# Performance work log

Measured on AMD Instinct MI355X. Metric: run time of the kernel, lower is better.

## Reference

```python
import jax, jax.numpy as jnp
import numpy as np


def _linear(x, W, b):
    # torch nn.Linear: y = x @ W.T + b, W is [out, in]
    return x @ W.T + b


def _sage_layer(x, edge_index, Ws, bs, Wn, bn):
    # GraphSAGE: mean-aggregate neighbor features via scatter-add, then two linears.
    src, tgt = edge_index[0], edge_index[1]
    N = x.shape[0]
    agg = jax.ops.segment_sum(x[src], tgt, num_segments=N)            # [N, D]
    deg = jax.ops.segment_sum(jnp.ones(src.shape, x.dtype), tgt, num_segments=N)  # [N]
    neighbor_mean = agg / jnp.maximum(deg, 1.0)[:, None]
    return _linear(x, Ws, bs) + _linear(neighbor_mean, Wn, bn)


def setup_inputs() -> dict:
    key = jax.random.key(0)
    ks = jax.random.split(key, 16)
    N, ATTR, H, OUT, E = 50000, 125, 128, 128, 800000
    IN = ATTR + 3
    s = 0.05
    inp = {
        "attr_features": jax.random.normal(ks[0], (N, ATTR), jnp.float32),
        "clustering_coefficient": jax.random.uniform(ks[1], (N, 1), jnp.float32),
        "bidirectional_links_ratio": jax.random.uniform(ks[2], (N, 1), jnp.float32),
        "exist_nodes": jnp.ones((N,), jnp.float32),
        "W_in": s * jax.random.normal(ks[3], (H, IN), jnp.float32),
        "b_in": s * jax.random.normal(ks[4], (H,), jnp.float32),
        "W1_self": s * jax.random.normal(ks[5], (H, H), jnp.float32),
        "b1_self": s * jax.random.normal(ks[6], (H,), jnp.float32),
        "W1_neigh": s * jax.random.normal(ks[7], (H, H), jnp.float32),
        "b1_neigh": s * jax.random.normal(ks[8], (H,), jnp.float32),
        "W2_self": s * jax.random.normal(ks[9], (OUT, H), jnp.float32),
        "b2_self": s * jax.random.normal(ks[10], (OUT,), jnp.float32),
        "W2_neigh": s * jax.random.normal(ks[11], (OUT, H), jnp.float32),
        "b2_neigh": s * jax.random.normal(ks[12], (OUT,), jnp.float32),
        "edge_index": jax.random.randint(ks[13], (2, E), 0, N, jnp.int64),
    }
    return inp


def reference(attr_features, clustering_coefficient, bidirectional_links_ratio,
              exist_nodes, W_in, b_in, W1_self, b1_self, W1_neigh, b1_neigh,
              W2_self, b2_self, W2_neigh, b2_neigh, edge_index):
    exist_col = exist_nodes[:, None]                                   # [N, 1]
    x = jnp.concatenate(
        [attr_features, clustering_coefficient, bidirectional_links_ratio, exist_col],
        axis=1)                                                        # [N, attr_dim+3]
    x = jax.nn.relu(_linear(x, W_in, b_in))                            # dropout=0 -> identity
    x = _sage_layer(x, edge_index, W1_self, b1_self, W1_neigh, b1_neigh)
    x = jax.nn.relu(x)
    x = x * exist_col
    x = _sage_layer(x, edge_index, W2_self, b2_self, W2_neigh, b2_neigh)
    return x * exist_col
```

## Files before the change

kernel.cpp:

```cpp
#include <hip/hip_runtime.h>

typedef __attribute__((ext_vector_type(8))) short short8;
typedef __attribute__((ext_vector_type(4))) float floatx4;

__device__ inline unsigned short f2bf(float f) {
    unsigned u = __float_as_uint(f);
    u += 0x7fffu + ((u >> 16) & 1u);
    return (unsigned short)(u >> 16);
}

#define CHUNK_CAP 12288
#define BTILE 4096
#define NPREP 256


__global__ __launch_bounds__(256, 3) void gemm0_bin(
    const float* __restrict__ attr, const float* __restrict__ cc,
    const float* __restrict__ bl, const float* __restrict__ ex,
    const float* __restrict__ Wf, const float* __restrict__ bias,
    unsigned short* __restrict__ out_bf,
    const int* __restrict__ e, int* __restrict__ cursor,
    unsigned* __restrict__ packed_out,
    const float* __restrict__ w1s, const float* __restrict__ w1n,
    const float* __restrict__ w2s, const float* __restrict__ w2n,
    const float* __restrict__ b1s, const float* __restrict__ b1n,
    const float* __restrict__ b2s, const float* __restrict__ b2n,
    unsigned short* __restrict__ wb, float* __restrict__ biasf,
    int N, int ATTR, int E, int ntilesE, int nbin) {
    __shared__ __align__(16) char smem[49408];
    int t = threadIdx.x;
    int bid = blockIdx.x;

    if (bid < nbin) {
        unsigned* buf  = (unsigned*)smem;
        unsigned* sbuf = buf + BTILE;
        int* hist  = (int*)(sbuf + BTILE);
        int* offs  = hist + 128;
        int* gbase = offs + 128;
        int* lcur  = gbase + 128;
        for (int tile = bid; tile < ntilesE; tile += nbin) {
            int e0 = tile * BTILE;
            int cnt = min(BTILE, E - e0);
            if (t < 128) hist[t] = 0;
            __syncthreads();
            for (int j = t; j < cnt; j += 256) {
                unsigned src = (unsigned)e[e0 + j];
                unsigned tgt = (unsigned)e[E + e0 + j];
                unsigned c = tgt >> 9;
                buf[j] = (c << 25) | (src << 9) | (tgt & 511u);
                atomicAdd(&hist[c], 1);
            }
            __syncthreads();
            if (t < 128) offs[t] = hist[t];
            __syncthreads();
            for (int o = 1; o < 128; o <<= 1) {
                int v = (t < 128 && t >= o) ? offs[t - o] : 0;
                __syncthreads();
                if (t < 128) offs[t] += v;
                __syncthreads();
            }
            if (t < 128) {
                int excl = offs[t] - hist[t];
                offs[t] = excl;
                lcur[t] = excl;
                gbase[t] = (hist[t] > 0) ? t * CHUNK_CAP + atomicAdd(&cursor[t], hist[t]) : 0;
            }
            __syncthreads();
            for (int j = t; j < cnt; j += 256) {
                unsigned v = buf[j];
                int c = v >> 25;
                int p = atomicAdd(&lcur[c], 1);
                sbuf[p] = v;
            }
            __syncthreads();
            int wv = t >> 6, lane = t & 63;
            for (int c = wv; c < 128; c += 4) {
                int n = hist[c], lo = offs[c], gb = gbase[c];
                for (int j = lane; j < n; j += 64)
                    packed_out[gb + j] = sbuf[lo + j];
            }
            __syncthreads();
        }
        return;
    }

    if (bid < nbin + NPREP) {
        int pb = bid - nbin;
        int idx = pb * 256 + t;
        int m = idx >> 14, j = idx & 16383;
        const float* src = (m == 0) ? w1s : (m == 1) ? w1n : (m == 2) ? w2s : w2n;
        wb[idx] = f2bf(src[j]);
        if (pb == 0 && t < 128) {
            biasf[t]       = b1s[t] + b1n[t];
            biasf[128 + t] = b2s[t] + b2n[t];
        }
        return;
    }

    float* sflat = (float*)smem;
    unsigned short* lx = (unsigned short*)(smem + 32000);
    int lane = t & 63;
    int w = t >> 6;
    int node0 = (bid - nbin - NPREP) * 64;
    int n_off = w * 32;
    int q = lane >> 4;
    int m16 = lane & 15;

    int nrow = N - node0; nrow = nrow > 64 ? 64 : (nrow < 0 ? 0 : nrow);
    int nelem = nrow * ATTR;
    {
        const float* abase = attr + (size_t)node0 * ATTR;
        int nv = nelem >> 2;
        const float4* src4 = (const float4*)abase;
        for (int i = t; i < nv; i += 256) ((float4*)sflat)[i] = src4[i];
        for (int i = (nv << 2) + t; i < nelem; i += 256) sflat[i] = abase[i];
    }

    short8 bf[2][4];
    #pragma unroll
    for (int nt = 0; nt < 2; ++nt)
        #pragma unroll
        for (int kk = 0; kk < 4; ++kk) {
            const float* p = Wf + (n_off + nt * 16 + m16) * 128 + kk * 32 + q * 8;
            float4 aa = *(const float4*)p, bb = *(const float4*)(p + 4);
            short8 r;
            r[0] = (short)f2bf(aa.x); r[1] = (short)f2bf(aa.y);
            r[2] = (short)f2bf(aa.z); r[3] = (short)f2bf(aa.w);
            r[4] = (short)f2bf(bb.x); r[5] = (short)f2bf(bb.y);
            r[6] = (short)f2bf(bb.z); r[7] = (short)f2bf(bb.w);
            bf[nt][kk] = r;
        }

    floatx4 acc[4][2];
    #pragma unroll
    for (int nt = 0; nt < 2; ++nt) {
        float bv = bias[n_off + nt * 16 + m16];
        floatx4 b4 = {bv, bv, bv, bv};
        #pragma unroll
        for (int mt = 0; mt < 4; ++mt) acc[mt][nt] = b4;
    }
    __syncthreads();

    for (int i = 0; i < 32; ++i) {
        int idx = t + 256 * i;
        int nd = idx >> 7, col = idx & 127;
        int row = node0 + nd;
        float v = 0.0f;
        if (row < N) {
            if (col < ATTR)           v = sflat[nd * ATTR + col];
            else if (col == ATTR)     v = cc[row];
            else if (col == ATTR + 1) v = bl[row];
            else                      v = ex[row];
        }
        lx[nd * 136 + col] = f2bf(v);
    }
    __syncthreads();

    #pragma unroll
    for (int kk = 0; kk < 4; ++kk) {
        short8 a[4];
        #pragma unroll
        for (int mt = 0; mt < 4; ++mt)
            a[mt] = *(const short8*)(lx + (mt * 16 + m16) * 136 + kk * 32 + q * 8);
        #pragma unroll
        for (int mt = 0; mt < 4; ++mt) {
            acc[mt][0] = __builtin_amdgcn_mfma_f32_16x16x32_bf16(a[mt], bf[0][kk], acc[mt][0], 0, 0, 0);
            acc[mt][1] = __builtin_amdgcn_mfma_f32_16x16x32_bf16(a[mt], bf[1][kk], acc[mt][1], 0, 0, 0);
        }
    }

    for (int mt = 0; mt < 4; ++mt) {
        int rbase = node0 + mt * 16 + q * 4;
        for (int r = 0; r < 4; ++r) {
            int rr = rbase + r;
            if (rr >= N) continue;
            for (int nt = 0; nt < 2; ++nt) {
                float v = fmaxf(acc[mt][nt][r], 0.0f);
                out_bf[(size_t)rr * 128 + n_off + nt * 16 + m16] = f2bf(v);
            }
        }
    }
}


__global__ __launch_bounds__(256) void chunk_csr(const unsigned* __restrict__ packed,
                                                 const int* __restrict__ cursor,
                                                 uint2* __restrict__ rows2,
                                                 int* __restrict__ colv, int N) {
    __shared__ int hist[512], offs[512], lcnt[512], pp[256];
    __shared__ int sbuf[CHUNK_CAP];
    int c = blockIdx.x;
    int base = c * CHUNK_CAP;
    int cnt = cursor[c];
    int t = threadIdx.x;
    hist[t] = 0;
    hist[t + 256] = 0;
    __syncthreads();
    for (int j = t; j < cnt; j += 256)
        atomicAdd(&hist[packed[base + j] & 511u], 1);
    __syncthreads();
    int a0 = hist[2 * t], a1 = hist[2 * t + 1];
    pp[t] = a0 + a1;
    __syncthreads();
    for (int o = 1; o < 256; o <<= 1) {
        int v = (t >= o) ? pp[t - o] : 0;
        __syncthreads();
        pp[t] += v;
        __syncthreads();
    }
    int excl = pp[t] - (a0 + a1);
    offs[2 * t] = excl;
    offs[2 * t + 1] = excl + a0;
    lcnt[2 * t] = 0;
    lcnt[2 * t + 1] = 0;
    __syncthreads();
    for (int j = t; j < 512; j += 256) {
        int node = c * 512 + j;
        if (node < N) {
            uint2 r;
            r.x = base + offs[j];
            r.y = base + offs[j] + hist[j];
            rows2[node] = r;
        }
    }
    for (int j = t; j < cnt; j += 256) {
        unsigned v = packed[base + j];
        int node = v & 511u;
        int p = offs[node] + atomicAdd(&lcnt[node], 1);
        sbuf[p] = (v >> 9) & 0xFFFFu;
    }
    __syncthreads();
    for (int j = t; j < cnt; j += 256) colv[base + j] = sbuf[j];
}


__global__ __launch_bounds__(256) void agg_mean(const unsigned short* __restrict__ x,
                                                const uint2* __restrict__ rows2,
                                                const int* __restrict__ colv,
                                                unsigned short* __restrict__ nm, int N) {
    int wid = (blockIdx.x * 256 + threadIdx.x) >> 6;
    int lane = threadIdx.x & 63;
    if (wid >= N) return;
    uint2 r = rows2[wid];
    int s0 = r.x, s1 = r.y;
    int deg = s1 - s0;
    int mn = deg < 64 ? deg : 64;
    int cvec = (lane < mn) ? colv[s0 + lane] : 0;
    int quarter = lane >> 4;
    int cl = (lane & 15) * 8;
    float a0 = 0.f, a1 = 0.f, a2 = 0.f, a3 = 0.f;
    float a4 = 0.f, a5 = 0.f, a6 = 0.f, a7 = 0.f;
    int lim = mn - 1;
    for (int j = 0; j < mn; j += 32) {
        uint4 v[8];
        #pragma unroll
        for (int u = 0; u < 8; ++u) {
            int ei = j + 4 * u + quarter;
            int idx = (ei <= lim) ? ei : lim;
            int s = __shfl(cvec, idx, 64);
            v[u] = *(const uint4*)(x + (size_t)s * 128 + cl);
        }
        #pragma unroll
        for (int u = 0; u < 8; ++u) {
            int ei = j + 4 * u + quarter;
            if (ei <= lim) {
                a0 += __uint_as_float(v[u].x << 16);
                a1 += __uint_as_float(v[u].x & 0xffff0000u);
                a2 += __uint_as_float(v[u].y << 16);
                a3 += __uint_as_float(v[u].y & 0xffff0000u);
                a4 += __uint_as_float(v[u].z << 16);
                a5 += __uint_as_float(v[u].z & 0xffff0000u);
                a6 += __uint_as_float(v[u].w << 16);
                a7 += __uint_as_float(v[u].w & 0xffff0000u);
            }
        }
    }
    for (int e = s0 + 64; e < s1; e += 4) {
        int ei = e + quarter;
        int idx = (ei < s1) ? ei : s1 - 1;
        int s = colv[idx];
        uint4 v = *(const uint4*)(x + (size_t)s * 128 + cl);
        if (ei < s1) {
            a0 += __uint_as_float(v.x << 16);
            a1 += __uint_as_float(v.x & 0xffff0000u);
            a2 += __uint_as_float(v.y << 16);
            a3 += __uint_as_float(v.y & 0xffff0000u);
            a4 += __uint_as_float(v.z << 16);
            a5 += __uint_as_float(v.z & 0xffff0000u);
            a6 += __uint_as_float(v.w << 16);
            a7 += __uint_as_float(v.w & 0xffff0000u);
        }
    }
    a0 += __shfl_xor(a0, 16, 64); a0 += __shfl_xor(a0, 32, 64);
    a1 += __shfl_xor(a1, 16, 64); a1 += __shfl_xor(a1, 32, 64);
    a2 += __shfl_xor(a2, 16, 64); a2 += __shfl_xor(a2, 32, 64);
    a3 += __shfl_xor(a3, 16, 64); a3 += __shfl_xor(a3, 32, 64);
    a4 += __shfl_xor(a4, 16, 64); a4 += __shfl_xor(a4, 32, 64);
    a5 += __shfl_xor(a5, 16, 64); a5 += __shfl_xor(a5, 32, 64);
    a6 += __shfl_xor(a6, 16, 64); a6 += __shfl_xor(a6, 32, 64);
    a7 += __shfl_xor(a7, 16, 64); a7 += __shfl_xor(a7, 32, 64);
    if (quarter == 0) {
        float inv = 1.0f / (float)(deg > 1 ? deg : 1);
        a0 *= inv; a1 *= inv; a2 *= inv; a3 *= inv;
        a4 *= inv; a5 *= inv; a6 *= inv; a7 *= inv;
        uint4 o;
        o.x = ((unsigned)f2bf(a1) << 16) | (unsigned)f2bf(a0);
        o.y = ((unsigned)f2bf(a3) << 16) | (unsigned)f2bf(a2);
        o.z = ((unsigned)f2bf(a5) << 16) | (unsigned)f2bf(a4);
        o.w = ((unsigned)f2bf(a7) << 16) | (unsigned)f2bf(a6);
        *(uint4*)(nm + (size_t)wid * 128 + cl) = o;
    }
}


__global__ __launch_bounds__(256, 3) void gemm_fused(
    const unsigned short* __restrict__ X0, const unsigned short* __restrict__ X1,
    const unsigned short* __restrict__ W0, const unsigned short* __restrict__ W1,
    const float* __restrict__ bias, const float* __restrict__ ex,
    unsigned short* __restrict__ obf, float* __restrict__ of32,
    int N, int relu) {
    __shared__ unsigned short lx[64 * 136];
    int tid = threadIdx.x;
    int lane = tid & 63;
    int w = tid >> 6;
    int node0 = blockIdx.x * 64;
    int n_off = w * 32;
    int q = lane >> 4;
    int m16 = lane & 15;

    short8 bf0[2][4], bf1[2][4];
    #pragma unroll
    for (int nt = 0; nt < 2; ++nt)
        #pragma unroll
        for (int kk = 0; kk < 4; ++kk) {
            bf0[nt][kk] = *(const short8*)(W0 + (n_off + nt * 16 + m16) * 128 + kk * 32 + q * 8);
            bf1[nt][kk] = *(const short8*)(W1 + (n_off + nt * 16 + m16) * 128 + kk * 32 + q * 8);
        }

    floatx4 acc[4][2];
    #pragma unroll
    for (int nt = 0; nt < 2; ++nt) {
        float bv = bias[n_off + nt * 16 + m16];
        floatx4 b4 = {bv, bv, bv, bv};
        #pragma unroll
        for (int mt = 0; mt < 4; ++mt) acc[mt][nt] = b4;
    }

    for (int ph = 0; ph < 2; ++ph) {
        const unsigned short* X = ph ? X1 : X0;
        for (int i = 0; i < 4; ++i) {
            int c = tid + 256 * i;
            int nd = c >> 4, ck = c & 15;
            short8 v = {0, 0, 0, 0, 0, 0, 0, 0};
            if (node0 + nd < N) v = *(const short8*)(X + (size_t)(node0 + nd) * 128 + ck * 8);
            *(short8*)(lx + nd * 136 + ck * 8) = v;
        }
        __syncthreads();
        #pragma unroll
        for (int kk = 0; kk < 4; ++kk) {
            short8 a[4];
            #pragma unroll
            for (int mt = 0; mt < 4; ++mt)
                a[mt] = *(const short8*)(lx + (mt * 16 + m16) * 136 + kk * 32 + q * 8);
            #pragma unroll
            for (int mt = 0; mt < 4; ++mt) {
                const short8* p0 = ph ? &bf1[0][kk] : &bf0[0][kk];
                const short8* p1 = ph ? &bf1[1][kk] : &bf0[1][kk];
                acc[mt][0] = __builtin_amdgcn_mfma_f32_16x16x32_bf16(a[mt], *p0, acc[mt][0], 0, 0, 0);
                acc[mt][1] = __builtin_amdgcn_mfma_f32_16x16x32_bf16(a[mt], *p1, acc[mt][1], 0, 0, 0);
            }
        }
        __syncthreads();
    }

    for (int mt = 0; mt < 4; ++mt) {
        int rbase = node0 + mt * 16 + q * 4;
        for (int r = 0; r < 4; ++r) {
            int rr = rbase + r;
            if (rr >= N) continue;
            float e = ex ? ex[rr] : 1.0f;
            for (int nt = 0; nt < 2; ++nt) {
                float v = acc[mt][nt][r];
                if (relu) v = fmaxf(v, 0.0f);
                v *= e;
                int col = n_off + nt * 16 + m16;
                if (obf) obf[(size_t)rr * 128 + col] = f2bf(v);
                else     of32[(size_t)rr * 128 + col] = v;
            }
        }
    }
}


extern "C" void kernel_launch(void* const* d_in, const int* in_sizes, int n_in,
                              void* d_out, int out_size, void* d_ws, size_t ws_size,
                              hipStream_t stream) {
    const float* attr = (const float*)d_in[0];
    const float* cc   = (const float*)d_in[1];
    const float* bl   = (const float*)d_in[2];
    const float* ex   = (const float*)d_in[3];
    const float* w_in = (const float*)d_in[4];
    const float* b_in = (const float*)d_in[5];
    const float* w1s  = (const float*)d_in[6];
    const float* b1s  = (const float*)d_in[7];
    const float* w1n  = (const float*)d_in[8];
    const float* b1n  = (const float*)d_in[9];
    const float* w2s  = (const float*)d_in[10];
    const float* b2s  = (const float*)d_in[11];
    const float* w2n  = (const float*)d_in[12];
    const float* b2n  = (const float*)d_in[13];
    const int*   eidx = (const int*)d_in[14];

    int N = in_sizes[3];
    int ATTR = in_sizes[0] / N;
    int E = in_sizes[14] / 2;
    int Npad = ((N + 63) / 64) * 64;
    int nchunk = (N + 511) / 512;
    int ntilesE = (E + BTILE - 1) / BTILE;
    int nbin = ntilesE < 256 ? ntilesE : 256;
    int gblk = Npad / 64;

    char* ws = (char*)d_ws;
    size_t off = 0;
    auto alloc = [&](size_t bytes) -> char* {
        off = (off + 255) & ~(size_t)255;
        char* p = ws + off;
        off += bytes;
        return p;
    };
    unsigned short* x1 = (unsigned short*)alloc((size_t)Npad * 128 * 2);
    unsigned short* x2 = (unsigned short*)alloc((size_t)Npad * 128 * 2);
    unsigned short* nm = (unsigned short*)alloc((size_t)Npad * 128 * 2);
    int* colv        = (int*)alloc((size_t)nchunk * CHUNK_CAP * 4);
    unsigned* packed = (unsigned*)alloc((size_t)nchunk * CHUNK_CAP * 4);
    uint2* rows2     = (uint2*)alloc((size_t)N * 8);
    int* cursor      = (int*)alloc(128 * 4);
    unsigned short* wb = (unsigned short*)alloc((size_t)4 * 16384 * 2);
    float* biasf     = (float*)alloc(256 * 4);

    hipMemsetAsync(cursor, 0, 128 * sizeof(int), stream);

    gemm0_bin<<<nbin + NPREP + gblk, 256, 0, stream>>>(
        attr, cc, bl, ex, w_in, b_in, x1,
        eidx, cursor, packed,
        w1s, w1n, w2s, w2n, b1s, b1n, b2s, b2n, wb, biasf,
        N, ATTR, E, ntilesE, nbin);
    chunk_csr<<<nchunk, 256, 0, stream>>>(packed, cursor, rows2, colv, N);
    agg_mean<<<(N + 3) / 4, 256, 0, stream>>>(x1, rows2, colv, nm, N);
    gemm_fused<<<gblk, 256, 0, stream>>>(x1, nm, wb, wb + 16384,
                                         biasf, ex, x2, (float*)nullptr, N, 1);
    agg_mean<<<(N + 3) / 4, 256, 0, stream>>>(x2, rows2, colv, nm, N);
    gemm_fused<<<gblk, 256, 0, stream>>>(x2, nm, wb + 2 * 16384, wb + 3 * 16384,
                                         biasf + 128, ex, (unsigned short*)nullptr,
                                         (float*)d_out, N, 0);
}
```

Baseline: 242.1 us.

## Fuse CSR build into front kernel and fuse neighbor aggregation into SAGE GEMMs

The chunk_csr pass moves into the front kernel, with CSR blocks spin-waiting on a global done counter set by the binning blocks. Binning now uses one 2048-edge tile per block instead of a grid-stride loop. Mean aggregation is computed inside each SAGE GEMM block straight into shared memory, which drops the nm buffer and three launches. The input GEMM now loads attr directly with vectorised loads, and outputs are staged through LDS for coalesced stores. The spin-wait relies on binning blocks being scheduled before the waiting blocks and adds some deadlock and ordering risk.

```diff
diff --git a/kernel.cpp b/kernel.cpp
--- a/kernel.cpp
+++ b/kernel.cpp
@@ -10,82 +10,134 @@
 }
 
 #define CHUNK_CAP 12288
-#define BTILE 4096
+#define BTILE 2048
 #define NPREP 256
 
 
-__global__ __launch_bounds__(256, 3) void gemm0_bin(
+__global__ __launch_bounds__(256, 4) void front_fused(
     const float* __restrict__ attr, const float* __restrict__ cc,
     const float* __restrict__ bl, const float* __restrict__ ex,
-    const float* __restrict__ Wf, const float* __restrict__ bias,
-    unsigned short* __restrict__ out_bf,
-    const int* __restrict__ e, int* __restrict__ cursor,
+    const float* __restrict__ Wf, const float* __restrict__ bias0,
+    unsigned short* __restrict__ x1,
+    const int* __restrict__ e, int* __restrict__ cursor, int* __restrict__ done,
     unsigned* __restrict__ packed_out,
+    uint2* __restrict__ rows2, int* __restrict__ colv,
     const float* __restrict__ w1s, const float* __restrict__ w1n,
     const float* __restrict__ w2s, const float* __restrict__ w2n,
     const float* __restrict__ b1s, const float* __restrict__ b1n,
     const float* __restrict__ b2s, const float* __restrict__ b2n,
     unsigned short* __restrict__ wb, float* __restrict__ biasf,
-    int N, int ATTR, int E, int ntilesE, int nbin) {
-    __shared__ __align__(16) char smem[49408];
+    int N, int ATTR, int E, int ntilesE, int nchunk) {
+    __shared__ __align__(16) char smem[18432];
     int t = threadIdx.x;
     int bid = blockIdx.x;
 
-    if (bid < nbin) {
+    if (bid < ntilesE) {
         unsigned* buf  = (unsigned*)smem;
         unsigned* sbuf = buf + BTILE;
         int* hist  = (int*)(sbuf + BTILE);
         int* offs  = hist + 128;
         int* gbase = offs + 128;
         int* lcur  = gbase + 128;
-        for (int tile = bid; tile < ntilesE; tile += nbin) {
-            int e0 = tile * BTILE;
-            int cnt = min(BTILE, E - e0);
-            if (t < 128) hist[t] = 0;
+        int e0 = bid * BTILE;
+        int cnt = min(BTILE, E - e0);
+        if (t < 128) hist[t] = 0;
+        __syncthreads();
+        for (int j = t; j < cnt; j += 256) {
+            unsigned src = (unsigned)e[e0 + j];
+            unsigned tgt = (unsigned)e[E + e0 + j];
+            unsigned c = tgt >> 9;
+            buf[j] = (c << 25) | (src << 9) | (tgt & 511u);
+            atomicAdd(&hist[c], 1);
+        }
+        __syncthreads();
+        if (t < 128) offs[t] = hist[t];
+        __syncthreads();
+        for (int o = 1; o < 128; o <<= 1) {
+            int v = (t < 128 && t >= o) ? offs[t - o] : 0;
             __syncthreads();
-            for (int j = t; j < cnt; j += 256) {
-                unsigned src = (unsigned)e[e0 + j];
-                unsigned tgt = (unsigned)e[E + e0 + j];
-                unsigned c = tgt >> 9;
-                buf[j] = (c << 25) | (src << 9) | (tgt & 511u);
-                atomicAdd(&hist[c], 1);
-            }
+            if (t < 128) offs[t] += v;
             __syncthreads();
-            if (t < 128) offs[t] = hist[t];
+        }
+        if (t < 128) {
+            int excl = offs[t] - hist[t];
+            offs[t] = excl;
+            lcur[t] = excl;
+            gbase[t] = (hist[t] > 0) ? t * CHUNK_CAP + atomicAdd(&cursor[t], hist[t]) : 0;
+        }
+        __syncthreads();
+        for (int j = t; j < cnt; j += 256) {
+            unsigned v = buf[j];
+            int c = v >> 25;
+            int p = atomicAdd(&lcur[c], 1);
+            sbuf[p] = v;
+        }
+        __syncthreads();
+        for (int j = t; j < cnt; j += 256) {
+            unsigned v = sbuf[j];
+            int c = v >> 25;
+            packed_out[gbase[c] + (j - offs[c])] = v;
+        }
+        __threadfence();
+        __syncthreads();
+        if (t == 0) atomicAdd(done, 1);
+        return;
+    }
+
+    if (bid < ntilesE + nchunk) {
+        int* hist = (int*)smem;
+        int* offs = hist + 512;
+        int* lcnt = offs + 512;
+        int* pp   = lcnt + 512;
+        int c = bid - ntilesE;
+        if (t == 0) {
+            while (atomicAdd(done, 0) < ntilesE) __builtin_amdgcn_s_sleep(8);
+            __threadfence();
+        }
+        __syncthreads();
+        int base = c * CHUNK_CAP;
+        int cnt = atomicAdd(&cursor[c], 0);
+        hist[t] = 0;
+        hist[t + 256] = 0;
+        __syncthreads();
+        for (int j = t; j < cnt; j += 256)
+            atomicAdd(&hist[packed_out[base + j] & 511u], 1);
+        __syncthreads();
+        int a0 = hist[2 * t], a1 = hist[2 * t + 1];
+        pp[t] = a0 + a1;
+        __syncthreads();
+        for (int o = 1; o < 256; o <<= 1) {
+            int v = (t >= o) ? pp[t - o] : 0;
             __syncthreads();
-            for (int o = 1; o < 128; o <<= 1) {
-                int v = (t < 128 && t >= o) ? offs[t - o] : 0;
-                __syncthreads();
-                if (t < 128) offs[t] += v;
-                __syncthreads();
-            }
-            if (t < 128) {
-                int excl = offs[t] - hist[t];
-                offs[t] = excl;
-                lcur[t] = excl;
-                gbase[t] = (hist[t] > 0) ? t * CHUNK_CAP + atomicAdd(&cursor[t], hist[t]) : 0;
-            }
+            pp[t] += v;
             __syncthreads();
-            for (int j = t; j < cnt; j += 256) {
-                unsigned v = buf[j];
-                int c = v >> 25;
-                int p = atomicAdd(&lcur[c], 1);
-                sbuf[p] = v;
-            }
-            __syncthreads();
-            int wv = t >> 6, lane = t & 63;
-            for (int c = wv; c < 128; c += 4) {
-                int n = hist[c], lo = offs[c], gb = gbase[c];
-                for (int j = lane; j < n; j += 64)
-                    packed_out[gb + j] = sbuf[lo + j];
-            }
-            __syncthreads();
+        }
+        int excl = pp[t] - (a0 + a1);
+        offs[2 * t] = excl;
+        offs[2 * t + 1] = excl + a0;
+        lcnt[2 * t] = 0;
+        lcnt[2 * t + 1] = 0;
+        __syncthreads();
+        for (int j = t; j < 512; j += 256) {
+            int node = c * 512 + j;
+            if (node < N) {
+                uint2 r;
+                r.x = base + offs[j];
+                r.y = base + offs[j] + hist[j];
+                rows2[node] = r;
+            }
+        }
+        for (int j = t; j < cnt; j += 256) {
+            unsigned v = packed_out[base + j];
+            int node = v & 511u;
+            int p = offs[node] + atomicAdd(&lcnt[node], 1);
+            colv[base + p] = (v >> 9) & 0xFFFFu;
         }
         return;
     }
 
-    if (bid < nbin + NPREP) {
-        int pb = bid - nbin;
+    if (bid < ntilesE + nchunk + NPREP) {
+        int pb = bid - ntilesE - nchunk;
         int idx = pb * 256 + t;
         int m = idx >> 14, j = idx & 16383;
         const float* src = (m == 0) ? w1s : (m == 1) ? w1n : (m == 2) ? w2s : w2n;
@@ -97,24 +149,13 @@
         return;
     }
 
-    float* sflat = (float*)smem;
-    unsigned short* lx = (unsigned short*)(smem + 32000);
+    unsigned short* lx = (unsigned short*)smem;
     int lane = t & 63;
     int w = t >> 6;
-    int node0 = (bid - nbin - NPREP) * 64;
+    int node0 = (bid - ntilesE - nchunk - NPREP) * 64;
     int n_off = w * 32;
     int q = lane >> 4;
     int m16 = lane & 15;
-
-    int nrow = N - node0; nrow = nrow > 64 ? 64 : (nrow < 0 ? 0 : nrow);
-    int nelem = nrow * ATTR;
-    {
-        const float* abase = attr + (size_t)node0 * ATTR;
-        int nv = nelem >> 2;
-        const float4* src4 = (const float4*)abase;
-        for (int i = t; i < nv; i += 256) ((float4*)sflat)[i] = src4[i];
-        for (int i = (nv << 2) + t; i < nelem; i += 256) sflat[i] = abase[i];
-    }
 
     short8 bf[2][4];
     #pragma unroll
@@ -134,25 +175,45 @@
     floatx4 acc[4][2];
     #pragma unroll
     for (int nt = 0; nt < 2; ++nt) {
-        float bv = bias[n_off + nt * 16 + m16];
+        float bv = bias0[n_off + nt * 16 + m16];
         floatx4 b4 = {bv, bv, bv, bv};
         #pragma unroll
         for (int mt = 0; mt < 4; ++mt) acc[mt][nt] = b4;
     }
-    __syncthreads();
-
-    for (int i = 0; i < 32; ++i) {
+
+    if (node0 + 64 > N) {
+        for (int i = t; i < 64 * 136; i += 256) lx[i] = 0;
+        __syncthreads();
+    }
+
+    #pragma unroll
+    for (int i = 0; i < 8; ++i) {
         int idx = t + 256 * i;
-        int nd = idx >> 7, col = idx & 127;
+        int nd = idx >> 5, g = idx & 31;
         int row = node0 + nd;
-        float v = 0.0f;
-        if (row < N) {
-            if (col < ATTR)           v = sflat[nd * ATTR + col];
-            else if (col == ATTR)     v = cc[row];
-            else if (col == ATTR + 1) v = bl[row];
-            else                      v = ex[row];
-        }
-        lx[nd * 136 + col] = f2bf(v);
+        int c0 = g * 4;
+        if (row < N && c0 < ATTR) {
+            if (c0 + 3 < ATTR) {
+                float4 f = *(const float4*)(attr + (size_t)row * ATTR + c0);
+                unsigned lo = (unsigned)f2bf(f.x) | ((unsigned)f2bf(f.y) << 16);
+                unsigned hi = (unsigned)f2bf(f.z) | ((unsigned)f2bf(f.w) << 16);
+                uint2 pk; pk.x = lo; pk.y = hi;
+                *(uint2*)(lx + nd * 136 + c0) = pk;
+            } else {
+                for (int k = 0; k < 4; ++k) {
+                    int cidx = c0 + k;
+                    if (cidx < ATTR) lx[nd * 136 + cidx] = f2bf(attr[(size_t)row * ATTR + cidx]);
+                }
+            }
+        }
+    }
+    {
+        int nd = t >> 2, ci = t & 3;
+        int row = node0 + nd;
+        if (ci < 3 && row < N) {
+            float v = (ci == 0) ? cc[row] : (ci == 1) ? bl[row] : ex[row];
+            lx[nd * 136 + ATTR + ci] = f2bf(v);
+        }
     }
     __syncthreads();
 
@@ -169,160 +230,41 @@
         }
     }
 
-    for (int mt = 0; mt < 4; ++mt) {
-        int rbase = node0 + mt * 16 + q * 4;
+    __syncthreads();
+    #pragma unroll
+    for (int mt = 0; mt < 4; ++mt)
+        #pragma unroll
         for (int r = 0; r < 4; ++r) {
-            int rr = rbase + r;
-            if (rr >= N) continue;
-            for (int nt = 0; nt < 2; ++nt) {
-                float v = fmaxf(acc[mt][nt][r], 0.0f);
-                out_bf[(size_t)rr * 128 + n_off + nt * 16 + m16] = f2bf(v);
-            }
-        }
+            int rl = mt * 16 + q * 4 + r;
+            #pragma unroll
+            for (int nt = 0; nt < 2; ++nt)
+                lx[rl * 136 + n_off + nt * 16 + m16] = f2bf(fmaxf(acc[mt][nt][r], 0.0f));
+        }
+    __syncthreads();
+    #pragma unroll
+    for (int i = 0; i < 4; ++i) {
+        int cidx = t + 256 * i;
+        int nd = cidx >> 4, k = cidx & 15;
+        int rr = node0 + nd;
+        if (rr < N)
+            *(uint4*)(x1 + (size_t)rr * 128 + k * 8) = *(const uint4*)(lx + nd * 136 + k * 8);
     }
 }
 
 
-__global__ __launch_bounds__(256) void chunk_csr(const unsigned* __restrict__ packed,
-                                                 const int* __restrict__ cursor,
-                                                 uint2* __restrict__ rows2,
-                                                 int* __restrict__ colv, int N) {
-    __shared__ int hist[512], offs[512], lcnt[512], pp[256];
-    __shared__ int sbuf[CHUNK_CAP];
-    int c = blockIdx.x;
-    int base = c * CHUNK_CAP;
-    int cnt = cursor[c];
-    int t = threadIdx.x;
-    hist[t] = 0;
-    hist[t + 256] = 0;
-    __syncthreads();
-    for (int j = t; j < cnt; j += 256)
-        atomicAdd(&hist[packed[base + j] & 511u], 1);
-    __syncthreads();
-    int a0 = hist[2 * t], a1 = hist[2 * t + 1];
-    pp[t] = a0 + a1;
-    __syncthreads();
-    for (int o = 1; o < 256; o <<= 1) {
-        int v = (t >= o) ? pp[t - o] : 0;
-        __syncthreads();
-        pp[t] += v;
-        __syncthreads();
-    }
-    int excl = pp[t] - (a0 + a1);
-    offs[2 * t] = excl;
-    offs[2 * t + 1] = excl + a0;
-    lcnt[2 * t] = 0;
-    lcnt[2 * t + 1] = 0;
-    __syncthreads();
-    for (int j = t; j < 512; j += 256) {
-        int node = c * 512 + j;
-        if (node < N) {
-            uint2 r;
-            r.x = base + offs[j];
-            r.y = base + offs[j] + hist[j];
-            rows2[node] = r;
-        }
-    }
-    for (int j = t; j < cnt; j += 256) {
-        unsigned v = packed[base + j];
-        int node = v & 511u;
-        int p = offs[node] + atomicAdd(&lcnt[node], 1);
-        sbuf[p] = (v >> 9) & 0xFFFFu;
-    }
-    __syncthreads();
-    for (int j = t; j < cnt; j += 256) colv[base + j] = sbuf[j];
-}
-
-
-__global__ __launch_bounds__(256) void agg_mean(const unsigned short* __restrict__ x,
-                                                const uint2* __restrict__ rows2,
-                                                const int* __restrict__ colv,
-                                                unsigned short* __restrict__ nm, int N) {
-    int wid = (blockIdx.x * 256 + threadIdx.x) >> 6;
-    int lane = threadIdx.x & 63;
-    if (wid >= N) return;
-    uint2 r = rows2[wid];
-    int s0 = r.x, s1 = r.y;
-    int deg = s1 - s0;
-    int mn = deg < 64 ? deg : 64;
-    int cvec = (lane < mn) ? colv[s0 + lane] : 0;
-    int quarter = lane >> 4;
-    int cl = (lane & 15) * 8;
-    float a0 = 0.f, a1 = 0.f, a2 = 0.f, a3 = 0.f;
-    float a4 = 0.f, a5 = 0.f, a6 = 0.f, a7 = 0.f;
-    int lim = mn - 1;
-    for (int j = 0; j < mn; j += 32) {
-        uint4 v[8];
-        #pragma unroll
-        for (int u = 0; u < 8; ++u) {
-            int ei = j + 4 * u + quarter;
-            int idx = (ei <= lim) ? ei : lim;
-            int s = __shfl(cvec, idx, 64);
-            v[u] = *(const uint4*)(x + (size_t)s * 128 + cl);
-        }
-        #pragma unroll
-        for (int u = 0; u < 8; ++u) {
-            int ei = j + 4 * u + quarter;
-            if (ei <= lim) {
-                a0 += __uint_as_float(v[u].x << 16);
-                a1 += __uint_as_float(v[u].x & 0xffff0000u);
-                a2 += __uint_as_float(v[u].y << 16);
-                a3 += __uint_as_float(v[u].y & 0xffff0000u);
-                a4 += __uint_as_float(v[u].z << 16);
-                a5 += __uint_as_float(v[u].z & 0xffff0000u);
-                a6 += __uint_as_float(v[u].w << 16);
-                a7 += __uint_as_float(v[u].w & 0xffff0000u);
-            }
-        }
-    }
-    for (int e = s0 + 64; e < s1; e += 4) {
-        int ei = e + quarter;
-        int idx = (ei < s1) ? ei : s1 - 1;
-        int s = colv[idx];
-        uint4 v = *(const uint4*)(x + (size_t)s * 128 + cl);
-        if (ei < s1) {
-            a0 += __uint_as_float(v.x << 16);
-            a1 += __uint_as_float(v.x & 0xffff0000u);
-            a2 += __uint_as_float(v.y << 16);
-            a3 += __uint_as_float(v.y & 0xffff0000u);
-            a4 += __uint_as_float(v.z << 16);
-            a5 += __uint_as_float(v.z & 0xffff0000u);
-            a6 += __uint_as_float(v.w << 16);
-            a7 += __uint_as_float(v.w & 0xffff0000u);
-        }
-    }
-    a0 += __shfl_xor(a0, 16, 64); a0 += __shfl_xor(a0, 32, 64);
-    a1 += __shfl_xor(a1, 16, 64); a1 += __shfl_xor(a1, 32, 64);
-    a2 += __shfl_xor(a2, 16, 64); a2 += __shfl_xor(a2, 32, 64);
-    a3 += __shfl_xor(a3, 16, 64); a3 += __shfl_xor(a3, 32, 64);
-    a4 += __shfl_xor(a4, 16, 64); a4 += __shfl_xor(a4, 32, 64);
-    a5 += __shfl_xor(a5, 16, 64); a5 += __shfl_xor(a5, 32, 64);
-    a6 += __shfl_xor(a6, 16, 64); a6 += __shfl_xor(a6, 32, 64);
-    a7 += __shfl_xor(a7, 16, 64); a7 += __shfl_xor(a7, 32, 64);
-    if (quarter == 0) {
-        float inv = 1.0f / (float)(deg > 1 ? deg : 1);
-        a0 *= inv; a1 *= inv; a2 *= inv; a3 *= inv;
-        a4 *= inv; a5 *= inv; a6 *= inv; a7 *= inv;
-        uint4 o;
-        o.x = ((unsigned)f2bf(a1) << 16) | (unsigned)f2bf(a0);
-        o.y = ((unsigned)f2bf(a3) << 16) | (unsigned)f2bf(a2);
-        o.z = ((unsigned)f2bf(a5) << 16) | (unsigned)f2bf(a4);
-        o.w = ((unsigned)f2bf(a7) << 16) | (unsigned)f2bf(a6);
-        *(uint4*)(nm + (size_t)wid * 128 + cl) = o;
-    }
-}
-
-
-__global__ __launch_bounds__(256, 3) void gemm_fused(
-    const unsigned short* __restrict__ X0, const unsigned short* __restrict__ X1,
+__global__ __launch_bounds__(256, 3) void gemm_sage(
+    const unsigned short* __restrict__ X,
+    const uint2* __restrict__ rows2, const int* __restrict__ colv,
     const unsigned short* __restrict__ W0, const unsigned short* __restrict__ W1,
     const float* __restrict__ bias, const float* __restrict__ ex,
     unsigned short* __restrict__ obf, float* __restrict__ of32,
     int N, int relu) {
-    __shared__ unsigned short lx[64 * 136];
-    int tid = threadIdx.x;
-    int lane = tid & 63;
-    int w = tid >> 6;
+    __shared__ __align__(16) char smem[34816];
+    unsigned short* lxA = (unsigned short*)smem;
+    unsigned short* lxB = lxA + 64 * 136;
+    int t = threadIdx.x;
+    int lane = t & 63;
+    int w = t >> 6;
     int node0 = blockIdx.x * 64;
     int n_off = w * 32;
     int q = lane >> 4;
@@ -346,47 +288,163 @@
         for (int mt = 0; mt < 4; ++mt) acc[mt][nt] = b4;
     }
 
-    for (int ph = 0; ph < 2; ++ph) {
-        const unsigned short* X = ph ? X1 : X0;
+    #pragma unroll
+    for (int i = 0; i < 4; ++i) {
+        int c = t + 256 * i;
+        int nd = c >> 4, ck = c & 15;
+        short8 v = {0, 0, 0, 0, 0, 0, 0, 0};
+        if (node0 + nd < N) v = *(const short8*)(X + (size_t)(node0 + nd) * 128 + ck * 8);
+        *(short8*)(lxA + nd * 136 + ck * 8) = v;
+    }
+
+    int cl = m16 * 8;
+    for (int i = 0; i < 16; ++i) {
+        int row = w * 16 + i;
+        int node = node0 + row;
+        int s0 = 0, s1 = 0;
+        if (node < N) { uint2 r2 = rows2[node]; s0 = r2.x; s1 = r2.y; }
+        int deg = s1 - s0;
+        int mn = deg < 64 ? deg : 64;
+        int cvec = (lane < mn) ? colv[s0 + lane] : 0;
+        float a0 = 0.f, a1 = 0.f, a2 = 0.f, a3 = 0.f;
+        float a4 = 0.f, a5 = 0.f, a6 = 0.f, a7 = 0.f;
+        int lim = mn - 1;
+        for (int j = 0; j < mn; j += 32) {
+            uint4 v[8];
+            #pragma unroll
+            for (int u = 0; u < 8; ++u) {
+                int ei = j + 4 * u + q;
+                int idx = (ei <= lim) ? ei : lim;
+                int s = __shfl(cvec, idx, 64);
+                v[u] = *(const uint4*)(X + (size_t)s * 128 + cl);
+            }
+            #pragma unroll
+            for (int u = 0; u < 8; ++u) {
+                int ei = j + 4 * u + q;
+                if (ei <= lim) {
+                    a0 += __uint_as_float(v[u].x << 16);
+                    a1 += __uint_as_float(v[u].x & 0xffff0000u);
+                    a2 += __uint_as_float(v[u].y << 16);
+                    a3 += __uint_as_float(v[u].y & 0xffff0000u);
+                    a4 += __uint_as_float(v[u].z << 16);
+                    a5 += __uint_as_float(v[u].z & 0xffff0000u);
+                    a6 += __uint_as_float(v[u].w << 16);
+                    a7 += __uint_as_float(v[u].w & 0xffff0000u);
+                }
+            }
+        }
+        for (int eo = s0 + 64; eo < s1; eo += 4) {
+            int ei = eo + q;
+            int idx = (ei < s1) ? ei : s1 - 1;
+            int s = colv[idx];
+            uint4 v = *(const uint4*)(X + (size_t)s * 128 + cl);
+            if (ei < s1) {
+                a0 += __uint_as_float(v.x << 16);
+                a1 += __uint_as_float(v.x & 0xffff0000u);
+                a2 += __uint_as_float(v.y << 16);
+                a3 += __uint_as_float(v.y & 0xffff0000u);
+                a4 += __uint_as_float(v.z << 16);
+                a5 += __uint_as_float(v.z & 0xffff0000u);
+                a6 += __uint_as_float(v.w << 16);
+                a7 += __uint_as_float(v.w & 0xffff0000u);
+            }
+        }
+        a0 += __shfl_xor(a0, 16, 64); a0 += __shfl_xor(a0, 32, 64);
+        a1 += __shfl_xor(a1, 16, 64); a1 += __shfl_xor(a1, 32, 64);
+        a2 += __shfl_xor(a2, 16, 64); a2 += __shfl_xor(a2, 32, 64);
+        a3 += __shfl_xor(a3, 16, 64); a3 += __shfl_xor(a3, 32, 64);
+        a4 += __shfl_xor(a4, 16, 64); a4 += __shfl_xor(a4, 32, 64);
+        a5 += __shfl_xor(a5, 16, 64); a5 += __shfl_xor(a5, 32, 64);
+        a6 += __shfl_xor(a6, 16, 64); a6 += __shfl_xor(a6, 32, 64);
+        a7 += __shfl_xor(a7, 16, 64); a7 += __shfl_xor(a7, 32, 64);
+        if (q == 0) {
+            float inv = 1.0f / (float)(deg > 1 ? deg : 1);
+            a0 *= inv; a1 *= inv; a2 *= inv; a3 *= inv;
+            a4 *= inv; a5 *= inv; a6 *= inv; a7 *= inv;
+            uint4 o;
+            o.x = ((unsigned)f2bf(a1) << 16) | (unsigned)f2bf(a0);
+            o.y = ((unsigned)f2bf(a3) << 16) | (unsigned)f2bf(a2);
+            o.z = ((unsigned)f2bf(a5) << 16) | (unsigned)f2bf(a4);
+            o.w = ((unsigned)f2bf(a7) << 16) | (unsigned)f2bf(a6);
+            *(uint4*)(lxB + row * 136 + cl) = o;
+        }
+    }
+    __syncthreads();
+
+    #pragma unroll
+    for (int kk = 0; kk < 4; ++kk) {
+        short8 a[4];
+        #pragma unroll
+        for (int mt = 0; mt < 4; ++mt)
+            a[mt] = *(const short8*)(lxA + (mt * 16 + m16) * 136 + kk * 32 + q * 8);
+        #pragma unroll
+        for (int mt = 0; mt < 4; ++mt) {
+            acc[mt][0] = __builtin_amdgcn_mfma_f32_16x16x32_bf16(a[mt], bf0[0][kk], acc[mt][0], 0, 0, 0);
+            acc[mt][1] = __builtin_amdgcn_mfma_f32_16x16x32_bf16(a[mt], bf0[1][kk], acc[mt][1], 0, 0, 0);
+        }
+    }
+    #pragma unroll
+    for (int kk = 0; kk < 4; ++kk) {
+        short8 a[4];
+        #pragma unroll
+        for (int mt = 0; mt < 4; ++mt)
+            a[mt] = *(const short8*)(lxB + (mt * 16 + m16) * 136 + kk * 32 + q * 8);
+        #pragma unroll
+        for (int mt = 0; mt < 4; ++mt) {
+            acc[mt][0] = __builtin_amdgcn_mfma_f32_16x16x32_bf16(a[mt], bf1[0][kk], acc[mt][0], 0, 0, 0);
+            acc[mt][1] = __builtin_amdgcn_mfma_f32_16x16x32_bf16(a[mt], bf1[1][kk], acc[mt][1], 0, 0, 0);
+        }
+    }
+    __syncthreads();
+
+    if (of32) {
+        float* C = (float*)smem;
+        #pragma unroll
+        for (int mt = 0; mt < 4; ++mt)
+            #pragma unroll
+            for (int r = 0; r < 4; ++r) {
+                int rl = mt * 16 + q * 4 + r;
+                int rr = node0 + rl;
+                float e = (rr < N && ex) ? ex[rr] : 0.0f;
+                #pragma unroll
+                for (int nt = 0; nt < 2; ++nt) {
+                    float v = acc[mt][nt][r];
+                    if (relu) v = fmaxf(v, 0.0f);
+                    C[rl * 132 + n_off + nt * 16 + m16] = v * e;
+                }
+            }
+        __syncthreads();
+        #pragma unroll
+        for (int i = 0; i < 8; ++i) {
+            int g = t + 256 * i;
+            int nd = g >> 5, k = g & 31;
+            int rr = node0 + nd;
+            if (rr < N)
+                *(float4*)(of32 + (size_t)rr * 128 + k * 4) = *(const float4*)(C + nd * 132 + k * 4);
+        }
+    } else {
+        #pragma unroll
+        for (int mt = 0; mt < 4; ++mt)
+            #pragma unroll
+            for (int r = 0; r < 4; ++r) {
+                int rl = mt * 16 + q * 4 + r;
+                int rr = node0 + rl;
+                float e = (rr < N && ex) ? ex[rr] : 0.0f;
+                #pragma unroll
+                for (int nt = 0; nt < 2; ++nt) {
+                    float v = acc[mt][nt][r];
+                    if (relu) v = fmaxf(v, 0.0f);
+                    lxA[rl * 136 + n_off + nt * 16 + m16] = f2bf(v * e);
+                }
+            }
+        __syncthreads();
+        #pragma unroll
         for (int i = 0; i < 4; ++i) {
-            int c = tid + 256 * i;
-            int nd = c >> 4, ck = c & 15;
-            short8 v = {0, 0, 0, 0, 0, 0, 0, 0};
-            if (node0 + nd < N) v = *(const short8*)(X + (size_t)(node0 + nd) * 128 + ck * 8);
-            *(short8*)(lx + nd * 136 + ck * 8) = v;
-        }
-        __syncthreads();
-        #pragma unroll
-        for (int kk = 0; kk < 4; ++kk) {
-            short8 a[4];
-            #pragma unroll
-            for (int mt = 0; mt < 4; ++mt)
-                a[mt] = *(const short8*)(lx + (mt * 16 + m16) * 136 + kk * 32 + q * 8);
-            #pragma unroll
-            for (int mt = 0; mt < 4; ++mt) {
-                const short8* p0 = ph ? &bf1[0][kk] : &bf0[0][kk];
-                const short8* p1 = ph ? &bf1[1][kk] : &bf0[1][kk];
-                acc[mt][0] = __builtin_amdgcn_mfma_f32_16x16x32_bf16(a[mt], *p0, acc[mt][0], 0, 0, 0);
-                acc[mt][1] = __builtin_amdgcn_mfma_f32_16x16x32_bf16(a[mt], *p1, acc[mt][1], 0, 0, 0);
-            }
-        }
-        __syncthreads();
-    }
-
-    for (int mt = 0; mt < 4; ++mt) {
-        int rbase = node0 + mt * 16 + q * 4;
-        for (int r = 0; r < 4; ++r) {
-            int rr = rbase + r;
-            if (rr >= N) continue;
-            float e = ex ? ex[rr] : 1.0f;
-            for (int nt = 0; nt < 2; ++nt) {
-                float v = acc[mt][nt][r];
-                if (relu) v = fmaxf(v, 0.0f);
-                v *= e;
-                int col = n_off + nt * 16 + m16;
-                if (obf) obf[(size_t)rr * 128 + col] = f2bf(v);
-                else     of32[(size_t)rr * 128 + col] = v;
-            }
+            int cidx = t + 256 * i;
+            int nd = cidx >> 4, k = cidx & 15;
+            int rr = node0 + nd;
+            if (rr < N)
+                *(uint4*)(obf + (size_t)rr * 128 + k * 8) = *(const uint4*)(lxA + nd * 136 + k * 8);
         }
     }
 }
@@ -417,7 +475,6 @@
     int Npad = ((N + 63) / 64) * 64;
     int nchunk = (N + 511) / 512;
     int ntilesE = (E + BTILE - 1) / BTILE;
-    int nbin = ntilesE < 256 ? ntilesE : 256;
     int gblk = Npad / 64;
 
     char* ws = (char*)d_ws;
@@ -430,27 +487,24 @@
     };
     unsigned short* x1 = (unsigned short*)alloc((size_t)Npad * 128 * 2);
     unsigned short* x2 = (unsigned short*)alloc((size_t)Npad * 128 * 2);
-    unsigned short* nm = (unsigned short*)alloc((size_t)Npad * 128 * 2);
     int* colv        = (int*)alloc((size_t)nchunk * CHUNK_CAP * 4);
     unsigned* packed = (unsigned*)alloc((size_t)nchunk * CHUNK_CAP * 4);
     uint2* rows2     = (uint2*)alloc((size_t)N * 8);
-    int* cursor      = (int*)alloc(128 * 4);
+    int* cursor      = (int*)alloc(132 * 4);
     unsigned short* wb = (unsigned short*)alloc((size_t)4 * 16384 * 2);
     float* biasf     = (float*)alloc(256 * 4);
-
-    hipMemsetAsync(cursor, 0, 128 * sizeof(int), stream);
-
-    gemm0_bin<<<nbin + NPREP + gblk, 256, 0, stream>>>(
+    int* done        = cursor + 128;
+
+    hipMemsetAsync(cursor, 0, 132 * sizeof(int), stream);
+
+    front_fused<<<ntilesE + nchunk + NPREP + gblk, 256, 0, stream>>>(
         attr, cc, bl, ex, w_in, b_in, x1,
-        eidx, cursor, packed,
+        eidx, cursor, done, packed, rows2, colv,
         w1s, w1n, w2s, w2n, b1s, b1n, b2s, b2n, wb, biasf,
-        N, ATTR, E, ntilesE, nbin);
-    chunk_csr<<<nchunk, 256, 0, stream>>>(packed, cursor, rows2, colv, N);
-    agg_mean<<<(N + 3) / 4, 256, 0, stream>>>(x1, rows2, colv, nm, N);
-    gemm_fused<<<gblk, 256, 0, stream>>>(x1, nm, wb, wb + 16384,
-                                         biasf, ex, x2, (float*)nullptr, N, 1);
-    agg_mean<<<(N + 3) / 4, 256, 0, stream>>>(x2, rows2, colv, nm, N);
-    gemm_fused<<<gblk, 256, 0, stream>>>(x2, nm, wb + 2 * 16384, wb + 3 * 16384,
-                                         biasf + 128, ex, (unsigned short*)nullptr,
-                                         (float*)d_out, N, 0);
+        N, ATTR, E, ntilesE, nchunk);
+    gemm_sage<<<gblk, 256, 0, stream>>>(x1, rows2, colv, wb, wb + 16384,
+                                        biasf, ex, x2, (float*)nullptr, N, 1);
+    gemm_sage<<<gblk, 256, 0, stream>>>(x2, rows2, colv, wb + 2 * 16384, wb + 3 * 16384,
+                                        biasf + 128, ex, (unsigned short*)nullptr,
+                                        (float*)d_out, N, 0);
 }
```

New measurement: 350.6 us. +44.8%, slower.
